# Optimization experiments

Hardware: AMD Instinct MI355X
Metric: run time of the kernel (lower is better)

## Reference

```python
import jax, jax.numpy as jnp
import numpy as np

REG1 = 0.5
REG2 = 0.5
ALPHA = 0.5

def setup_inputs() -> dict:
    key = jax.random.key(0)
    k1, k2, k3, k4, k5 = jax.random.split(key, 5)
    N, D, K = 32768, 256, 2048
    return {
        "encoder_out": jax.random.normal(k1, (N, D), dtype=jnp.float32),
        "prototypes": jax.random.normal(k2, (K, D), dtype=jnp.float32),
        "recon_loss": jax.random.uniform(k3, (), dtype=jnp.float32),
        "kl_loss": jax.random.uniform(k4, (), dtype=jnp.float32),
        "mmd_loss": jax.random.uniform(k5, (), dtype=jnp.float32),
    }


def _cdist_min_loss(z, prototypes):
    # torch.cdist(z, protos) -> [N, K]; f_dist = cdist(protos, z) = its transpose.
    # prototypes accessed via .data in torch -> detached.
    p = jax.lax.stop_gradient(prototypes)
    z2 = jnp.sum(z * z, axis=1, keepdims=True)          # [N, 1]
    p2 = jnp.sum(p * p, axis=1)                          # [K]
    sq = z2 + p2[None, :] - 2.0 * (z @ p.T)              # [N, K]
    dist = jnp.sqrt(jnp.maximum(sq, 0.0))
    p_min = jnp.min(dist, axis=1).mean()   # p_dist.min(1).values.mean()
    f_min = jnp.min(dist, axis=0).mean()   # f_dist [K,N].min(1) == dist.min(0)
    return REG1 * p_min + REG2 * f_min


def reference(encoder_out, prototypes, recon_loss, kl_loss, mmd_loss):
    cvae_loss = recon_loss + ALPHA * kl_loss + mmd_loss
    prot_decoding_loss = _cdist_min_loss(encoder_out, prototypes)
    # no projection head (use_projector=False)
    x = encoder_out / jnp.maximum(
        jnp.linalg.norm(encoder_out, axis=1, keepdims=True), 1e-12)
    x_mapped = x @ prototypes.T  # [N, K]
    return (encoder_out, x, x_mapped, cvae_loss, prot_decoding_loss)
```

## Files before the change

### kernel.cpp

```cpp
#include <hip/hip_runtime.h>
#include <hip/hip_bf16.h>

typedef __bf16 bf16x8 __attribute__((ext_vector_type(8)));
typedef __bf16 bf16x4 __attribute__((ext_vector_type(4)));
typedef float  f32x4  __attribute__((ext_vector_type(4)));

#define N_ROWS 32768
#define D_DIM  256
#define K_PROT 2048

#define WS_Z2    0
#define WS_INVN  32768
#define WS_P2    65536
#define WS_RMIN  67584
#define WS_CMIN  100352
#define WS_ZB    102400
#define WS_PB    (102400 + 4194304)

#define OUT_X0   0UL
#define OUT_X1   8388608UL
#define OUT_XMAP 16777216UL
#define OUT_CVAE 83886080UL
#define OUT_PROT 83886081UL

__device__ __forceinline__ void gload16(const __bf16* gsrc, const __bf16* ldst) {
    auto g = (const __attribute__((address_space(1))) unsigned int*)(unsigned long long)gsrc;
    auto l = (__attribute__((address_space(3))) unsigned int*)(unsigned long long)ldst;
    __builtin_amdgcn_global_load_lds(g, l, 16, 0, 0);
}

__global__ __launch_bounds__(256) void k1_rows(
    const float* __restrict__ Z, float* __restrict__ out0, float* __restrict__ out1,
    float* __restrict__ z2, float* __restrict__ invn, unsigned int* __restrict__ rmin,
    __bf16* __restrict__ Zb)
{
    int row  = (blockIdx.x << 2) + (threadIdx.x >> 6);
    int lane = threadIdx.x & 63;
    size_t base = (size_t)row * D_DIM;
    float4 v = ((const float4*)(Z + base))[lane];
    float ss = v.x*v.x + v.y*v.y + v.z*v.z + v.w*v.w;
    #pragma unroll
    for (int d = 32; d >= 1; d >>= 1) ss += __shfl_xor(ss, d);
    float inv = 1.0f / fmaxf(sqrtf(ss), 1e-12f);
    ((float4*)(out0 + base))[lane] = v;
    float4 xv; xv.x = v.x*inv; xv.y = v.y*inv; xv.z = v.z*inv; xv.w = v.w*inv;
    ((float4*)(out1 + base))[lane] = xv;
    bf16x4 bv; bv[0]=(__bf16)v.x; bv[1]=(__bf16)v.y; bv[2]=(__bf16)v.z; bv[3]=(__bf16)v.w;
    ((bf16x4*)(Zb + base))[lane] = bv;
    if (lane == 0) { z2[row] = ss; invn[row] = inv; rmin[row] = 0x7f800000u; }
}

__global__ __launch_bounds__(256) void k2_prot(
    const float* __restrict__ P, float* __restrict__ p2, unsigned int* __restrict__ cmin,
    __bf16* __restrict__ Pb)
{
    int row  = (blockIdx.x << 2) + (threadIdx.x >> 6);
    int lane = threadIdx.x & 63;
    size_t base = (size_t)row * D_DIM;
    float4 v = ((const float4*)(P + base))[lane];
    float ss = v.x*v.x + v.y*v.y + v.z*v.z + v.w*v.w;
    #pragma unroll
    for (int d = 32; d >= 1; d >>= 1) ss += __shfl_xor(ss, d);
    bf16x4 bv; bv[0]=(__bf16)v.x; bv[1]=(__bf16)v.y; bv[2]=(__bf16)v.z; bv[3]=(__bf16)v.w;
    ((bf16x4*)(Pb + base))[lane] = bv;
    if (lane == 0) { p2[row] = ss; cmin[row] = 0x7f800000u; }
}

#define BM 128
#define BN 128
#define BK 64

__global__ __launch_bounds__(256, 2) void k3_gemm(
    const __bf16* __restrict__ Zb, const __bf16* __restrict__ Pb,
    const float* __restrict__ z2, const float* __restrict__ p2,
    const float* __restrict__ invn,
    float* __restrict__ xmap,
    unsigned int* __restrict__ rmin, unsigned int* __restrict__ cmin)
{
    __shared__ __bf16 As[BM * BK];
    __shared__ __bf16 Bs[BN * BK];

    const int tid  = threadIdx.x;
    const int bn   = blockIdx.x & 15;
    const int bm   = blockIdx.x >> 4;
    const int lane = tid & 63;
    const int wave = tid >> 6;
    const int wm   = wave >> 1;
    const int wn   = wave & 1;
    const int l15  = lane & 15;
    const int quad = lane >> 4;

    const int m0 = bm * BM;
    const int n0 = bn * BN;

    f32x4 acc[4][4];
    #pragma unroll
    for (int i = 0; i < 4; i++)
        #pragma unroll
        for (int j = 0; j < 4; j++)
            #pragma unroll
            for (int r = 0; r < 4; r++) acc[i][j][r] = 0.0f;

    const int ch_row[4] = {
        ((0*4 + wave)*64 + lane) >> 3, ((1*4 + wave)*64 + lane) >> 3,
        ((2*4 + wave)*64 + lane) >> 3, ((3*4 + wave)*64 + lane) >> 3 };
    const int ch_c = lane & 7;

    for (int kt = 0; kt < D_DIM; kt += BK) {
        #pragma unroll
        for (int it = 0; it < 4; it++) {
            const __bf16* aS = Zb + (size_t)(m0 + ch_row[it]) * D_DIM + kt + ch_c * 8;
            const __bf16* bS = Pb + (size_t)(n0 + ch_row[it]) * D_DIM + kt + ch_c * 8;
            gload16(aS, As + (it*4 + wave) * 512);
            gload16(bS, Bs + (it*4 + wave) * 512);
        }
        __syncthreads();

        #pragma unroll
        for (int s = 0; s < 2; s++) {
            bf16x8 af[4], bfr[4];
            #pragma unroll
            for (int i = 0; i < 4; i++)
                af[i] = *(const bf16x8*)(As + (wm*64 + i*16 + l15) * BK + s*32 + quad*8);
            #pragma unroll
            for (int j = 0; j < 4; j++)
                bfr[j] = *(const bf16x8*)(Bs + (wn*64 + j*16 + l15) * BK + s*32 + quad*8);
            #pragma unroll
            for (int i = 0; i < 4; i++)
                #pragma unroll
                for (int j = 0; j < 4; j++)
                    acc[i][j] = __builtin_amdgcn_mfma_f32_16x16x32_bf16(af[i], bfr[j], acc[i][j], 0, 0, 0);
        }
        __syncthreads();
    }

    float invr[16], zzr[16];
    #pragma unroll
    for (int i = 0; i < 4; i++)
        #pragma unroll
        for (int r = 0; r < 4; r++) {
            int gm = m0 + wm*64 + i*16 + quad*4 + r;
            invr[i*4+r] = invn[gm];
            zzr[i*4+r]  = z2[gm];
        }
    float pp[4];
    #pragma unroll
    for (int j = 0; j < 4; j++) pp[j] = p2[n0 + wn*64 + j*16 + l15];

    float cminv[4] = {3.0e38f, 3.0e38f, 3.0e38f, 3.0e38f};

    #pragma unroll
    for (int i = 0; i < 4; i++) {
        #pragma unroll
        for (int r = 0; r < 4; r++) {
            int gm = m0 + wm*64 + i*16 + quad*4 + r;
            float zi = zzr[i*4+r], iv = invr[i*4+r];
            size_t orow = (size_t)gm * K_PROT + n0 + wn*64 + l15;
            float rv = 3.0e38f;
            #pragma unroll
            for (int j = 0; j < 4; j++) {
                float g = acc[i][j][r];
                xmap[orow + j*16] = g * iv;
                float d = sqrtf(fmaxf(zi + pp[j] - 2.0f*g, 0.0f));
                rv = fminf(rv, d);
                cminv[j] = fminf(cminv[j], d);
            }
            #pragma unroll
            for (int s = 1; s < 16; s <<= 1) rv = fminf(rv, __shfl_xor(rv, s));
            if (l15 == 0) atomicMin(&rmin[gm], __float_as_uint(rv));
        }
    }
    #pragma unroll
    for (int j = 0; j < 4; j++) {
        float cv = cminv[j];
        cv = fminf(cv, __shfl_xor(cv, 16));
        cv = fminf(cv, __shfl_xor(cv, 32));
        if (quad == 0) atomicMin(&cmin[n0 + wn*64 + j*16 + l15], __float_as_uint(cv));
    }
}

__global__ __launch_bounds__(1024) void k4_final(
    const float* __restrict__ rminf, const float* __restrict__ cminf,
    const float* __restrict__ recon, const float* __restrict__ kl,
    const float* __restrict__ mmd, float* __restrict__ out)
{
    __shared__ float sr[16], sc[16];
    int tid = threadIdx.x;
    float a = 0.0f, b = 0.0f;
    for (int i = tid; i < N_ROWS; i += 1024) a += rminf[i];
    for (int i = tid; i < K_PROT; i += 1024) b += cminf[i];
    #pragma unroll
    for (int d = 32; d >= 1; d >>= 1) { a += __shfl_xor(a, d); b += __shfl_xor(b, d); }
    int w = tid >> 6, lane = tid & 63;
    if (lane == 0) { sr[w] = a; sc[w] = b; }
    __syncthreads();
    if (tid == 0) {
        float SA = 0.0f, SB = 0.0f;
        #pragma unroll
        for (int i = 0; i < 16; i++) { SA += sr[i]; SB += sc[i]; }
        out[OUT_CVAE] = recon[0] + 0.5f*kl[0] + mmd[0];
        out[OUT_PROT] = 0.5f*(SA / (float)N_ROWS) + 0.5f*(SB / (float)K_PROT);
    }
}

extern "C" void kernel_launch(void* const* d_in, const int* in_sizes, int n_in,
                              void* d_out, int out_size, void* d_ws, size_t ws_size,
                              hipStream_t stream)
{
    const float* Z     = (const float*)d_in[0];
    const float* P     = (const float*)d_in[1];
    const float* recon = (const float*)d_in[2];
    const float* kl    = (const float*)d_in[3];
    const float* mmd   = (const float*)d_in[4];
    float* out = (float*)d_out;
    float* ws  = (float*)d_ws;

    float* z2   = ws + WS_Z2;
    float* invn = ws + WS_INVN;
    float* p2   = ws + WS_P2;
    unsigned int* rmin = (unsigned int*)(ws + WS_RMIN);
    unsigned int* cmin = (unsigned int*)(ws + WS_CMIN);
    __bf16* Zb = (__bf16*)(ws + WS_ZB);
    __bf16* Pb = (__bf16*)(ws + WS_PB);

    hipLaunchKernelGGL(k1_rows, dim3(N_ROWS/4), dim3(256), 0, stream,
                       Z, out + OUT_X0, out + OUT_X1, z2, invn, rmin, Zb);
    hipLaunchKernelGGL(k2_prot, dim3(K_PROT/4), dim3(256), 0, stream, P, p2, cmin, Pb);
    hipLaunchKernelGGL(k3_gemm, dim3((N_ROWS/BM)*(K_PROT/BN)), dim3(256), 0, stream,
                       Zb, Pb, z2, p2, invn, out + OUT_XMAP, rmin, cmin);
    hipLaunchKernelGGL(k4_final, dim3(1), dim3(1024), 0, stream,
                       (const float*)rmin, (const float*)cmin, recon, kl, mmd, out);
}
```

Measured before the change: 428.3 us.

## Fuse prep kernels, remap GEMM blocks across XCDs, defer sqrt to final reduce

Merges the row-prep and prototype-prep kernels into one launch, which removes one kernel launch. Remaps GEMM workgroup indices so consecutive tiles land on the same XCD for better L2 reuse. Moves the sqrt out of the GEMM epilogue by taking mins on squared distances and applying sqrt only in the final reduction, which is valid because sqrt is monotone. This cuts transcendental work in the epilogue, at the cost of slightly more complex indexing.

```diff
diff --git a/kernel.cpp b/kernel.cpp
--- a/kernel.cpp
+++ b/kernel.cpp
@@ -29,41 +29,40 @@
     __builtin_amdgcn_global_load_lds(g, l, 16, 0, 0);
 }
 
-__global__ __launch_bounds__(256) void k1_rows(
-    const float* __restrict__ Z, float* __restrict__ out0, float* __restrict__ out1,
+__global__ __launch_bounds__(256) void k12_rows(
+    const float* __restrict__ Z, const float* __restrict__ P,
+    float* __restrict__ out0, float* __restrict__ out1,
     float* __restrict__ z2, float* __restrict__ invn, unsigned int* __restrict__ rmin,
-    __bf16* __restrict__ Zb)
-{
-    int row  = (blockIdx.x << 2) + (threadIdx.x >> 6);
+    __bf16* __restrict__ Zb,
+    float* __restrict__ p2, unsigned int* __restrict__ cmin, __bf16* __restrict__ Pb)
+{
+    int b    = blockIdx.x;
     int lane = threadIdx.x & 63;
-    size_t base = (size_t)row * D_DIM;
-    float4 v = ((const float4*)(Z + base))[lane];
-    float ss = v.x*v.x + v.y*v.y + v.z*v.z + v.w*v.w;
-    #pragma unroll
-    for (int d = 32; d >= 1; d >>= 1) ss += __shfl_xor(ss, d);
-    float inv = 1.0f / fmaxf(sqrtf(ss), 1e-12f);
-    ((float4*)(out0 + base))[lane] = v;
-    float4 xv; xv.x = v.x*inv; xv.y = v.y*inv; xv.z = v.z*inv; xv.w = v.w*inv;
-    ((float4*)(out1 + base))[lane] = xv;
-    bf16x4 bv; bv[0]=(__bf16)v.x; bv[1]=(__bf16)v.y; bv[2]=(__bf16)v.z; bv[3]=(__bf16)v.w;
-    ((bf16x4*)(Zb + base))[lane] = bv;
-    if (lane == 0) { z2[row] = ss; invn[row] = inv; rmin[row] = 0x7f800000u; }
-}
-
-__global__ __launch_bounds__(256) void k2_prot(
-    const float* __restrict__ P, float* __restrict__ p2, unsigned int* __restrict__ cmin,
-    __bf16* __restrict__ Pb)
-{
-    int row  = (blockIdx.x << 2) + (threadIdx.x >> 6);
-    int lane = threadIdx.x & 63;
-    size_t base = (size_t)row * D_DIM;
-    float4 v = ((const float4*)(P + base))[lane];
-    float ss = v.x*v.x + v.y*v.y + v.z*v.z + v.w*v.w;
-    #pragma unroll
-    for (int d = 32; d >= 1; d >>= 1) ss += __shfl_xor(ss, d);
-    bf16x4 bv; bv[0]=(__bf16)v.x; bv[1]=(__bf16)v.y; bv[2]=(__bf16)v.z; bv[3]=(__bf16)v.w;
-    ((bf16x4*)(Pb + base))[lane] = bv;
-    if (lane == 0) { p2[row] = ss; cmin[row] = 0x7f800000u; }
+    if (b < (N_ROWS/4)) {
+        int row  = (b << 2) + (threadIdx.x >> 6);
+        size_t base = (size_t)row * D_DIM;
+        float4 v = ((const float4*)(Z + base))[lane];
+        float ss = v.x*v.x + v.y*v.y + v.z*v.z + v.w*v.w;
+        #pragma unroll
+        for (int d = 32; d >= 1; d >>= 1) ss += __shfl_xor(ss, d);
+        float inv = 1.0f / fmaxf(sqrtf(ss), 1e-12f);
+        ((float4*)(out0 + base))[lane] = v;
+        float4 xv; xv.x = v.x*inv; xv.y = v.y*inv; xv.z = v.z*inv; xv.w = v.w*inv;
+        ((float4*)(out1 + base))[lane] = xv;
+        bf16x4 bv; bv[0]=(__bf16)v.x; bv[1]=(__bf16)v.y; bv[2]=(__bf16)v.z; bv[3]=(__bf16)v.w;
+        ((bf16x4*)(Zb + base))[lane] = bv;
+        if (lane == 0) { z2[row] = ss; invn[row] = inv; rmin[row] = 0x7f800000u; }
+    } else {
+        int row  = ((b - (N_ROWS/4)) << 2) + (threadIdx.x >> 6);
+        size_t base = (size_t)row * D_DIM;
+        float4 v = ((const float4*)(P + base))[lane];
+        float ss = v.x*v.x + v.y*v.y + v.z*v.z + v.w*v.w;
+        #pragma unroll
+        for (int d = 32; d >= 1; d >>= 1) ss += __shfl_xor(ss, d);
+        bf16x4 bv; bv[0]=(__bf16)v.x; bv[1]=(__bf16)v.y; bv[2]=(__bf16)v.z; bv[3]=(__bf16)v.w;
+        ((bf16x4*)(Pb + base))[lane] = bv;
+        if (lane == 0) { p2[row] = ss; cmin[row] = 0x7f800000u; }
+    }
 }
 
 #define BM 128
@@ -81,8 +80,9 @@
     __shared__ __bf16 Bs[BN * BK];
 
     const int tid  = threadIdx.x;
-    const int bn   = blockIdx.x & 15;
-    const int bm   = blockIdx.x >> 4;
+    const int wg   = (blockIdx.x & 7) * 512 + (blockIdx.x >> 3);
+    const int bn   = wg & 15;
+    const int bm   = wg >> 4;
     const int lane = tid & 63;
     const int wave = tid >> 6;
     const int wm   = wave >> 1;
@@ -161,9 +161,9 @@
             for (int j = 0; j < 4; j++) {
                 float g = acc[i][j][r];
                 xmap[orow + j*16] = g * iv;
-                float d = sqrtf(fmaxf(zi + pp[j] - 2.0f*g, 0.0f));
-                rv = fminf(rv, d);
-                cminv[j] = fminf(cminv[j], d);
+                float d2 = fmaxf(zi + pp[j] - 2.0f*g, 0.0f);
+                rv = fminf(rv, d2);
+                cminv[j] = fminf(cminv[j], d2);
             }
             #pragma unroll
             for (int s = 1; s < 16; s <<= 1) rv = fminf(rv, __shfl_xor(rv, s));
@@ -187,8 +187,8 @@
     __shared__ float sr[16], sc[16];
     int tid = threadIdx.x;
     float a = 0.0f, b = 0.0f;
-    for (int i = tid; i < N_ROWS; i += 1024) a += rminf[i];
-    for (int i = tid; i < K_PROT; i += 1024) b += cminf[i];
+    for (int i = tid; i < N_ROWS; i += 1024) a += sqrtf(fmaxf(rminf[i], 0.0f));
+    for (int i = tid; i < K_PROT; i += 1024) b += sqrtf(fmaxf(cminf[i], 0.0f));
     #pragma unroll
     for (int d = 32; d >= 1; d >>= 1) { a += __shfl_xor(a, d); b += __shfl_xor(b, d); }
     int w = tid >> 6, lane = tid & 63;
@@ -223,9 +223,8 @@
     __bf16* Zb = (__bf16*)(ws + WS_ZB);
     __bf16* Pb = (__bf16*)(ws + WS_PB);
 
-    hipLaunchKernelGGL(k1_rows, dim3(N_ROWS/4), dim3(256), 0, stream,
-                       Z, out + OUT_X0, out + OUT_X1, z2, invn, rmin, Zb);
-    hipLaunchKernelGGL(k2_prot, dim3(K_PROT/4), dim3(256), 0, stream, P, p2, cmin, Pb);
+    hipLaunchKernelGGL(k12_rows, dim3(N_ROWS/4 + K_PROT/4), dim3(256), 0, stream,
+                       Z, P, out + OUT_X0, out + OUT_X1, z2, invn, rmin, Zb, p2, cmin, Pb);
     hipLaunchKernelGGL(k3_gemm, dim3((N_ROWS/BM)*(K_PROT/BN)), dim3(256), 0, stream,
                        Zb, Pb, z2, p2, invn, out + OUT_XMAP, rmin, cmin);
     hipLaunchKernelGGL(k4_final, dim3(1), dim3(1024), 0, stream,
```

Result: slower. 437.3 us (+2.1%).
